# Kernel optimization log

Measured on AMD Instinct MI355X. Metric: run time of the kernel, lower is better.

The kernel has to match this reference:

```python
import jax, jax.numpy as jnp
import numpy as np

B, TQ, TK, QD, KD = 16, 256, 256, 512, 512

def setup_inputs() -> dict:
    key = jax.random.key(0)
    k = jax.random.split(key, 8)
    query = jax.random.normal(k[0], (B, TQ, QD), dtype=jnp.float32)
    keys = jax.random.normal(k[1], (B, TK, KD), dtype=jnp.float32)
    # linear_q: query_size -> key_size (stored as [in, out] for x @ W)
    Wq = jax.random.normal(k[2], (QD, KD), dtype=jnp.float32) * 0.02
    bq = jnp.zeros((KD,), dtype=jnp.float32)
    # linear_att: key_size -> 1
    w_att = jax.random.normal(k[3], (KD,), dtype=jnp.float32) * 0.02
    b_att = jnp.zeros((), dtype=jnp.float32)
    # linear_out: (query_size + key_size) -> query_size
    Wout = jax.random.normal(k[4], (QD + KD, QD), dtype=jnp.float32) * 0.02
    bout = jnp.zeros((QD,), dtype=jnp.float32)
    return {"query": query, "keys": keys, "Wq": Wq, "bq": bq,
            "w_att": w_att, "b_att": b_att, "Wout": Wout, "bout": bout}

def reference(query, keys, Wq, bq, w_att, b_att, Wout, bout):
    # att_query = linear_q(query): [b, t_q, n]
    att_query = query @ Wq + bq
    # Bahdanau additive score: tanh(q_i + k_j) . w + b  -> [b, t_q, t_k]
    sum_qk = jnp.tanh(att_query[:, :, None, :] + keys[:, None, :, :])  # b,tq,tk,n
    scores = jnp.einsum('bqkn,n->bqk', sum_qk, w_att) + b_att
    p = jax.nn.softmax(scores, axis=-1)  # softmax over t_k
    # values defaults to keys
    context = jnp.einsum('bqk,bkn->bqn', p, keys)
    # output transform: tanh(linear_out([query; context]))
    context = jnp.tanh(jnp.concatenate([query, context], axis=-1) @ Wout + bout)
    return context, p
```

## Files before the change

### kernel.cpp

```cpp
#include <hip/hip_runtime.h>


#define C2 2.88539008177792681f

typedef unsigned short u16;
typedef short s16x8 __attribute__((ext_vector_type(8)));
typedef float f32x4 __attribute__((ext_vector_type(4)));
typedef float f32x2 __attribute__((ext_vector_type(2)));

__device__ __forceinline__ float fast_rcp(float x) { return __builtin_amdgcn_rcpf(x); }
__device__ __forceinline__ f32x2 fma2(f32x2 a, f32x2 b, f32x2 c) {
  return __builtin_elementwise_fma(a, b, c);
}

__device__ __forceinline__ u16 f2bf(float f) {
  union { float f; unsigned u; } v; v.f = f;
  unsigned r = v.u + 0x7fffu + ((v.u >> 16) & 1u);
  return (u16)(r >> 16);
}
__device__ __forceinline__ unsigned packbf(float a, float b) {
  return (unsigned)f2bf(a) | ((unsigned)f2bf(b) << 16);
}

__global__ __launch_bounds__(256) void mega_prep(
    const float* __restrict__ keys, float* __restrict__ Ek,
    const float* __restrict__ query, u16* __restrict__ qbf,
    u16* __restrict__ kbfT,
    const float* __restrict__ Wq, u16* __restrict__ Wqt,
    const float* __restrict__ Wout, u16* __restrict__ Woutt,
    const float* __restrict__ w_att, const float* __restrict__ b_att,
    float* __restrict__ Cptr)
{
  __shared__ float red[4];
  __shared__ u16 tile[32][40];
  const int t = threadIdx.x;
  const int bx = blockIdx.x;

  if (bx < 2048) {
    const int b = bx >> 7, rem = bx & 127;
    const int k0 = (rem >> 4) * 32, n0 = (rem & 15) * 32;
    const float* src = keys + (size_t)b * 131072;
    const int r = t >> 3, c = (t & 7) * 4;
    const size_t off = (size_t)(k0 + r) * 512 + n0 + c;
    float4 v = *(const float4*)&src[off];
    float4 o;
    o.x = exp2f(C2 * v.x); o.y = exp2f(C2 * v.y);
    o.z = exp2f(C2 * v.z); o.w = exp2f(C2 * v.w);
    *(float4*)&Ek[(size_t)b * 131072 + off] = o;
    tile[c + 0][r] = f2bf(v.x); tile[c + 1][r] = f2bf(v.y);
    tile[c + 2][r] = f2bf(v.z); tile[c + 3][r] = f2bf(v.w);
    __syncthreads();
    if (t < 128) {
      const int row = t >> 2, ch = (t & 3) * 8;
      unsigned p0 = (unsigned)tile[row][ch + 0] | ((unsigned)tile[row][ch + 1] << 16);
      unsigned p1 = (unsigned)tile[row][ch + 2] | ((unsigned)tile[row][ch + 3] << 16);
      unsigned p2 = (unsigned)tile[row][ch + 4] | ((unsigned)tile[row][ch + 5] << 16);
      unsigned p3 = (unsigned)tile[row][ch + 6] | ((unsigned)tile[row][ch + 7] << 16);
      *(int4*)&kbfT[(size_t)b * 131072 + (size_t)(n0 + row) * 256 + k0 + ch] =
          make_int4(p0, p1, p2, p3);
    }
  } else if (bx < 3072) {
    const size_t i8 = ((size_t)(bx - 2048) * 256 + t) * 8;
    float4 a = *(const float4*)&query[i8];
    float4 b = *(const float4*)&query[i8 + 4];
    unsigned p0 = packbf(a.x, a.y), p1 = packbf(a.z, a.w);
    unsigned p2 = packbf(b.x, b.y), p3 = packbf(b.z, b.w);
    *(int4*)&qbf[i8] = make_int4(p0, p1, p2, p3);
  } else if (bx < 3840) {
    const int b3 = bx - 3072;
    const int by = b3 >> 4;
    const int n0 = (b3 & 15) * 32;
    const float* W; u16* Wt; int K, k0;
    if (by < 16) { W = Wq;   Wt = Wqt;   K = 512;  k0 = by * 32; }
    else         { W = Wout; Wt = Woutt; K = 1024; k0 = (by - 16) * 32; }
    const int r = t >> 3, c = (t & 7) * 4;
    float4 v = *(const float4*)&W[(size_t)(k0 + r) * 512 + n0 + c];
    tile[c + 0][r] = f2bf(v.x); tile[c + 1][r] = f2bf(v.y);
    tile[c + 2][r] = f2bf(v.z); tile[c + 3][r] = f2bf(v.w);
    __syncthreads();
    if (t < 128) {
      const int row = t >> 2, ch = (t & 3) * 8;
      unsigned p0 = (unsigned)tile[row][ch + 0] | ((unsigned)tile[row][ch + 1] << 16);
      unsigned p1 = (unsigned)tile[row][ch + 2] | ((unsigned)tile[row][ch + 3] << 16);
      unsigned p2 = (unsigned)tile[row][ch + 4] | ((unsigned)tile[row][ch + 5] << 16);
      unsigned p3 = (unsigned)tile[row][ch + 6] | ((unsigned)tile[row][ch + 7] << 16);
      *(int4*)&Wt[(size_t)(n0 + row) * K + k0 + ch] = make_int4(p0, p1, p2, p3);
    }
  } else {
    float wsum = w_att[t] + w_att[t + 256];
#pragma unroll
    for (int m = 32; m; m >>= 1) wsum += __shfl_xor(wsum, m);
    if ((t & 63) == 0) red[t >> 6] = wsum;
    __syncthreads();
    if (t == 0) Cptr[0] = red[0] + red[1] + red[2] + red[3] + b_att[0];
  }
}

__global__ __launch_bounds__(256) void gemm_mfma_bf16(
    const u16* __restrict__ A0, const u16* __restrict__ A1, int kSplit,
    const u16* __restrict__ Bt, const float* __restrict__ bias,
    float* __restrict__ C, int K, int act)
{
  __shared__ u16 As[64 * 72];
  __shared__ u16 Bs[64 * 72];
  const int t = threadIdx.x;
  const int lane = t & 63, wid = t >> 6;
  const int wm = wid >> 1, wn = wid & 1;
  const int col0 = blockIdx.x * 64, row0 = blockIdx.y * 64;
  const int lr = t >> 2, lc = (t & 3) * 16;
  const int fr = lane & 15, fg = (lane >> 4) * 8;

  f32x4 acc[2][2] = {};
  const int nIter = K >> 6;

  int4 a0v, a1v, b0v, b1v;
  {
    const u16* Asrc = (0 < kSplit) ? A0 : A1;
    a0v = *(const int4*)&Asrc[(size_t)(row0 + lr) * 512 + lc];
    a1v = *(const int4*)&Asrc[(size_t)(row0 + lr) * 512 + lc + 8];
    b0v = *(const int4*)&Bt[(size_t)(col0 + lr) * K + lc];
    b1v = *(const int4*)&Bt[(size_t)(col0 + lr) * K + lc + 8];
  }
  for (int it = 0; it < nIter; ++it) {
    __syncthreads();
    *(int4*)&As[lr * 72 + lc]     = a0v;
    *(int4*)&As[lr * 72 + lc + 8] = a1v;
    *(int4*)&Bs[lr * 72 + lc]     = b0v;
    *(int4*)&Bs[lr * 72 + lc + 8] = b1v;
    __syncthreads();

    if (it + 1 < nIter) {
      const int k0 = (it + 1) << 6;
      const u16* Asrc; int kc;
      if (k0 < kSplit) { Asrc = A0; kc = k0; } else { Asrc = A1; kc = k0 - kSplit; }
      a0v = *(const int4*)&Asrc[(size_t)(row0 + lr) * 512 + kc + lc];
      a1v = *(const int4*)&Asrc[(size_t)(row0 + lr) * 512 + kc + lc + 8];
      b0v = *(const int4*)&Bt[(size_t)(col0 + lr) * K + k0 + lc];
      b1v = *(const int4*)&Bt[(size_t)(col0 + lr) * K + k0 + lc + 8];
    }

#pragma unroll
    for (int ks = 0; ks < 2; ++ks) {
      s16x8 af[2], bf[2];
#pragma unroll
      for (int m = 0; m < 2; ++m)
        af[m] = *(const s16x8*)&As[(wm * 32 + m * 16 + fr) * 72 + ks * 32 + fg];
#pragma unroll
      for (int n = 0; n < 2; ++n)
        bf[n] = *(const s16x8*)&Bs[(wn * 32 + n * 16 + fr) * 72 + ks * 32 + fg];
#pragma unroll
      for (int m = 0; m < 2; ++m)
#pragma unroll
        for (int n = 0; n < 2; ++n)
          acc[m][n] = __builtin_amdgcn_mfma_f32_16x16x32_bf16(af[m], bf[n], acc[m][n], 0, 0, 0);
    }
  }

  const int fq = lane >> 4;
#pragma unroll
  for (int n = 0; n < 2; ++n) {
    const int col = col0 + wn * 32 + n * 16 + fr;
    const float bv = bias[col];
#pragma unroll
    for (int m = 0; m < 2; ++m) {
#pragma unroll
      for (int i = 0; i < 4; ++i) {
        const int row = row0 + wm * 32 + m * 16 + fq * 4 + i;
        float v = acc[m][n][i] + bv;
        if (act == 1) {
          float e = __expf(2.0f * v);
          v = 1.0f - 2.0f * fast_rcp(e + 1.0f);
        } else if (act == 2) {
          v = exp2f(C2 * v);
        }
        C[(size_t)row * 512 + col] = v;
      }
    }
  }
}

__global__ __launch_bounds__(256) void score_kernel(
    const float* __restrict__ Ea, const float* __restrict__ Ek,
    const float* __restrict__ w_att, const float* __restrict__ Cptr,
    float* __restrict__ S)
{
  __shared__ float ea_s[64][68];
  __shared__ float ek_s[64][68];

  const int z = blockIdx.z;
  const int b = z >> 2, qt = z & 3;
  const int q0 = blockIdx.y * 64, k0 = blockIdx.x * 64;
  const int t = threadIdx.x;

  const int qi = t >> 4, ki = t & 15;
  const int lr = t >> 2, lc = (t & 3) * 16;
  const float* eap = Ea + (size_t)(b * 256 + q0) * 512 + qt * 128;
  const float* ekp = Ek + (size_t)(b * 256 + k0) * 512 + qt * 128;
  const float* wbase = w_att + qt * 128;

  float acc[4][4] = {};
  const f32x2 one = {1.0f, 1.0f};

  for (int c = 0; c < 2; ++c) {
    const int gb = lr * 512 + c * 64 + lc;
    float4 A0 = *(const float4*)&eap[gb + 0];
    float4 A1 = *(const float4*)&eap[gb + 4];
    float4 A2 = *(const float4*)&eap[gb + 8];
    float4 A3 = *(const float4*)&eap[gb + 12];
    float4 K0 = *(const float4*)&ekp[gb + 0];
    float4 K1 = *(const float4*)&ekp[gb + 4];
    float4 K2 = *(const float4*)&ekp[gb + 8];
    float4 K3 = *(const float4*)&ekp[gb + 12];
    __syncthreads();
    *(float4*)&ea_s[lr][lc + 0]  = A0;
    *(float4*)&ea_s[lr][lc + 4]  = A1;
    *(float4*)&ea_s[lr][lc + 8]  = A2;
    *(float4*)&ea_s[lr][lc + 12] = A3;
    *(float4*)&ek_s[lr][lc + 0]  = K0;
    *(float4*)&ek_s[lr][lc + 4]  = K1;
    *(float4*)&ek_s[lr][lc + 8]  = K2;
    *(float4*)&ek_s[lr][lc + 12] = K3;
    __syncthreads();

    for (int j = 0; j < 64; j += 8) {
      f32x2 kp[4][4];
#pragma unroll
      for (int n = 0; n < 4; ++n) {
        float4 kv0 = *(const float4*)&ek_s[ki + n * 16][j];
        float4 kv1 = *(const float4*)&ek_s[ki + n * 16][j + 4];
        kp[n][0] = f32x2{kv0.x, kv0.y};
        kp[n][1] = f32x2{kv0.z, kv0.w};
        kp[n][2] = f32x2{kv1.x, kv1.y};
        kp[n][3] = f32x2{kv1.z, kv1.w};
      }
      const float* wq = wbase + c * 64 + j;
      f32x2 wp0 = {wq[0], wq[1]};
      f32x2 wp1 = {wq[2], wq[3]};
      f32x2 wp2 = {wq[4], wq[5]};
      f32x2 wp3 = {wq[6], wq[7]};

#pragma unroll
      for (int m = 0; m < 4; ++m) {
        float4 av0 = *(const float4*)&ea_s[qi + m * 16][j];
        float4 av1 = *(const float4*)&ea_s[qi + m * 16][j + 4];
        f32x2 ap0 = {av0.x, av0.y};
        f32x2 ap1 = {av0.z, av0.w};
        f32x2 ap2 = {av1.x, av1.y};
        f32x2 ap3 = {av1.z, av1.w};
#pragma unroll
        for (int n = 0; n < 4; ++n) {
          f32x2 q1 = fma2(ap0, kp[n][0], one);
          f32x2 q2 = fma2(ap1, kp[n][1], one);
          f32x2 q3 = fma2(ap2, kp[n][2], one);
          f32x2 q4 = fma2(ap3, kp[n][3], one);
          f32x2 N12 = fma2(wp0, q2, wp1 * q1);
          f32x2 D12 = q1 * q2;
          f32x2 N34 = fma2(wp2, q4, wp3 * q3);
          f32x2 D34 = q3 * q4;
          f32x2 Nt = fma2(N12, D34, N34 * D12);
          f32x2 Dt = D12 * D34;
          float r0 = fast_rcp(Dt.x);
          float r1 = fast_rcp(Dt.y);
          acc[m][n] = fmaf(Nt.x, r0, acc[m][n]);
          acc[m][n] = fmaf(Nt.y, r1, acc[m][n]);
        }
      }
    }
  }

  const float Cv = (qt == 0) ? Cptr[0] : 0.0f;
  float* sc = S + (size_t)qt * 1048576;
#pragma unroll
  for (int m = 0; m < 4; ++m) {
    const size_t qr = (size_t)(b * 256 + q0 + qi + m * 16);
#pragma unroll
    for (int n = 0; n < 4; ++n)
      sc[qr * 256 + k0 + ki + n * 16] = fmaf(-2.f, acc[m][n], Cv);
  }
}

__global__ __launch_bounds__(256) void softmax_kernel(
    const float* __restrict__ S, float* __restrict__ p_out,
    u16* __restrict__ pbf)
{
  const int t = threadIdx.x;
  const int w = t >> 6, lane = t & 63;
  const int row = blockIdx.x * 4 + w;
  const size_t off = (size_t)row * 256 + lane * 4;
  float4 sa = *(const float4*)&S[off];
  float4 sb = *(const float4*)&S[off + 1048576];
  float4 sc = *(const float4*)&S[off + 2097152];
  float4 sd = *(const float4*)&S[off + 3145728];
  float4 s4 = {(sa.x + sb.x) + (sc.x + sd.x), (sa.y + sb.y) + (sc.y + sd.y),
               (sa.z + sb.z) + (sc.z + sd.z), (sa.w + sb.w) + (sc.w + sd.w)};
  float m = fmaxf(fmaxf(s4.x, s4.y), fmaxf(s4.z, s4.w));
#pragma unroll
  for (int msk = 32; msk; msk >>= 1) m = fmaxf(m, __shfl_xor(m, msk));
  float e0 = __expf(s4.x - m);
  float e1 = __expf(s4.y - m);
  float e2 = __expf(s4.z - m);
  float e3 = __expf(s4.w - m);
  float ssum = (e0 + e1) + (e2 + e3);
#pragma unroll
  for (int msk = 32; msk; msk >>= 1) ssum += __shfl_xor(ssum, msk);
  float rs = 1.0f / ssum;
  float4 p4 = {e0 * rs, e1 * rs, e2 * rs, e3 * rs};
  *(float4*)&p_out[off] = p4;
  unsigned lo = packbf(p4.x, p4.y), hi = packbf(p4.z, p4.w);
  *(int2*)&pbf[off] = make_int2(lo, hi);
}

__global__ __launch_bounds__(256) void ctx_gemm(
    const u16* __restrict__ pbf, const u16* __restrict__ kbfT,
    u16* __restrict__ ctxbf)
{
  __shared__ u16 As[64 * 72];
  __shared__ u16 Bs[64 * 72];
  const int t = threadIdx.x;
  const int lane = t & 63, wid = t >> 6;
  const int wm = wid >> 1, wn = wid & 1;
  const int col0 = blockIdx.x * 64, row0 = blockIdx.y * 64, b = blockIdx.z;
  const u16* A = pbf + (size_t)b * 65536;
  const u16* Bm = kbfT + (size_t)b * 131072;
  const int lr = t >> 2, lc = (t & 3) * 16;
  const int fr = lane & 15, fg = (lane >> 4) * 8;

  f32x4 acc[2][2] = {};

  int4 a0v = *(const int4*)&A[(size_t)(row0 + lr) * 256 + lc];
  int4 a1v = *(const int4*)&A[(size_t)(row0 + lr) * 256 + lc + 8];
  int4 b0v = *(const int4*)&Bm[(size_t)(col0 + lr) * 256 + lc];
  int4 b1v = *(const int4*)&Bm[(size_t)(col0 + lr) * 256 + lc + 8];

  for (int it = 0; it < 4; ++it) {
    __syncthreads();
    *(int4*)&As[lr * 72 + lc]     = a0v;
    *(int4*)&As[lr * 72 + lc + 8] = a1v;
    *(int4*)&Bs[lr * 72 + lc]     = b0v;
    *(int4*)&Bs[lr * 72 + lc + 8] = b1v;
    __syncthreads();

    if (it < 3) {
      const int k0 = (it + 1) << 6;
      a0v = *(const int4*)&A[(size_t)(row0 + lr) * 256 + k0 + lc];
      a1v = *(const int4*)&A[(size_t)(row0 + lr) * 256 + k0 + lc + 8];
      b0v = *(const int4*)&Bm[(size_t)(col0 + lr) * 256 + k0 + lc];
      b1v = *(const int4*)&Bm[(size_t)(col0 + lr) * 256 + k0 + lc + 8];
    }

#pragma unroll
    for (int ks = 0; ks < 2; ++ks) {
      s16x8 af[2], bf[2];
#pragma unroll
      for (int m = 0; m < 2; ++m)
        af[m] = *(const s16x8*)&As[(wm * 32 + m * 16 + fr) * 72 + ks * 32 + fg];
#pragma unroll
      for (int n = 0; n < 2; ++n)
        bf[n] = *(const s16x8*)&Bs[(wn * 32 + n * 16 + fr) * 72 + ks * 32 + fg];
#pragma unroll
      for (int m = 0; m < 2; ++m)
#pragma unroll
        for (int n = 0; n < 2; ++n)
          acc[m][n] = __builtin_amdgcn_mfma_f32_16x16x32_bf16(af[m], bf[n], acc[m][n], 0, 0, 0);
    }
  }

  const int fq = lane >> 4;
#pragma unroll
  for (int n = 0; n < 2; ++n) {
    const int col = col0 + wn * 32 + n * 16 + fr;
#pragma unroll
    for (int m = 0; m < 2; ++m) {
#pragma unroll
      for (int i = 0; i < 4; ++i) {
        const int row = row0 + wm * 32 + m * 16 + fq * 4 + i;
        ctxbf[(size_t)(b * 256 + row) * 512 + col] = f2bf(acc[m][n][i]);
      }
    }
  }
}

extern "C" void kernel_launch(void* const* d_in, const int* in_sizes, int n_in,
                              void* d_out, int out_size, void* d_ws, size_t ws_size,
                              hipStream_t stream) {
  const float* query = (const float*)d_in[0];
  const float* keys  = (const float*)d_in[1];
  const float* Wq    = (const float*)d_in[2];
  const float* bq    = (const float*)d_in[3];
  const float* w_att = (const float*)d_in[4];
  const float* b_att = (const float*)d_in[5];
  const float* Wout  = (const float*)d_in[6];
  const float* bout  = (const float*)d_in[7];

  float* out_tanh = (float*)d_out;
  float* out_p    = out_tanh + (size_t)4096 * 512;

  float* ws = (float*)d_ws;
  float* Ea     = ws;
  float* Ek     = ws + 2097152;
  float* S      = ws + 4194304;
  float* Cptr   = ws + 8388608;
  u16*   Wqt    = (u16*)(ws + 8388624);
  u16*   Woutt  = Wqt + 262144;
  u16*   qbf    = Woutt + 524288;
  u16*   kbfT   = qbf + 2097152;
  u16*   pbf    = kbfT + 2097152;
  u16*   ctxbf  = (u16*)Ea;

  mega_prep<<<3841, 256, 0, stream>>>(
      keys, Ek, query, qbf, kbfT, Wq, Wqt, Wout, Woutt, w_att, b_att, Cptr);

  gemm_mfma_bf16<<<dim3(8, 64), 256, 0, stream>>>(
      qbf, qbf, 512, Wqt, bq, Ea, 512, 2);

  score_kernel<<<dim3(4, 4, 64), 256, 0, stream>>>(
      Ea, Ek, w_att, Cptr, S);

  softmax_kernel<<<1024, 256, 0, stream>>>(S, out_p, pbf);

  ctx_gemm<<<dim3(8, 4, 16), 256, 0, stream>>>(pbf, kbfT, ctxbf);

  gemm_mfma_bf16<<<dim3(8, 64), 256, 0, stream>>>(
      qbf, ctxbf, 512, Woutt, bout, out_tanh, 1024, 1);
}
```

Baseline: 100.2 us.

## Read query-side tiles directly from global memory and drop packed-float math in score kernel

The score kernel no longer stages the Ea (exp of projected query) tile in shared memory; each thread reads its query rows straight from global memory (relying on cache) while keys stay in LDS. The packed f32x2 arithmetic is replaced by scalar fmaf expressed through a macro, and w_att is loaded as float4. This cuts LDS traffic and shared-memory footprint, which may raise occupancy, at the cost of uncoalesced global loads and the loss of packed-FMA throughput on the dominant transcendental-free inner loop.

```diff
diff --git a/kernel.cpp b/kernel.cpp
--- a/kernel.cpp
+++ b/kernel.cpp
@@ -6,12 +6,8 @@
 typedef unsigned short u16;
 typedef short s16x8 __attribute__((ext_vector_type(8)));
 typedef float f32x4 __attribute__((ext_vector_type(4)));
-typedef float f32x2 __attribute__((ext_vector_type(2)));
 
 __device__ __forceinline__ float fast_rcp(float x) { return __builtin_amdgcn_rcpf(x); }
-__device__ __forceinline__ f32x2 fma2(f32x2 a, f32x2 b, f32x2 c) {
-  return __builtin_elementwise_fma(a, b, c);
-}
 
 __device__ __forceinline__ u16 f2bf(float f) {
   union { float f; unsigned u; } v; v.f = f;
@@ -184,7 +180,6 @@
     const float* __restrict__ w_att, const float* __restrict__ Cptr,
     float* __restrict__ S)
 {
-  __shared__ float ea_s[64][68];
   __shared__ float ek_s[64][68];
 
   const int z = blockIdx.z;
@@ -194,28 +189,32 @@
 
   const int qi = t >> 4, ki = t & 15;
   const int lr = t >> 2, lc = (t & 3) * 16;
-  const float* eap = Ea + (size_t)(b * 256 + q0) * 512 + qt * 128;
+  const float* eaq = Ea + (size_t)(b * 256 + q0 + qi) * 512 + qt * 128;
   const float* ekp = Ek + (size_t)(b * 256 + k0) * 512 + qt * 128;
   const float* wbase = w_att + qt * 128;
 
   float acc[4][4] = {};
-  const f32x2 one = {1.0f, 1.0f};
+
+#define TERM4(a4, kv, wv, accv) { \
+    float q1 = fmaf(a4.x, kv.x, 1.0f); \
+    float q2 = fmaf(a4.y, kv.y, 1.0f); \
+    float q3 = fmaf(a4.z, kv.z, 1.0f); \
+    float q4 = fmaf(a4.w, kv.w, 1.0f); \
+    float N12 = fmaf(wv.x, q2, wv.y * q1); \
+    float D12 = q1 * q2; \
+    float N34 = fmaf(wv.z, q4, wv.w * q3); \
+    float D34 = q3 * q4; \
+    float Nt = fmaf(N12, D34, N34 * D12); \
+    float Dt = D12 * D34; \
+    accv = fmaf(Nt, fast_rcp(Dt), accv); }
 
   for (int c = 0; c < 2; ++c) {
     const int gb = lr * 512 + c * 64 + lc;
-    float4 A0 = *(const float4*)&eap[gb + 0];
-    float4 A1 = *(const float4*)&eap[gb + 4];
-    float4 A2 = *(const float4*)&eap[gb + 8];
-    float4 A3 = *(const float4*)&eap[gb + 12];
     float4 K0 = *(const float4*)&ekp[gb + 0];
     float4 K1 = *(const float4*)&ekp[gb + 4];
     float4 K2 = *(const float4*)&ekp[gb + 8];
     float4 K3 = *(const float4*)&ekp[gb + 12];
     __syncthreads();
-    *(float4*)&ea_s[lr][lc + 0]  = A0;
-    *(float4*)&ea_s[lr][lc + 4]  = A1;
-    *(float4*)&ea_s[lr][lc + 8]  = A2;
-    *(float4*)&ea_s[lr][lc + 12] = A3;
     *(float4*)&ek_s[lr][lc + 0]  = K0;
     *(float4*)&ek_s[lr][lc + 4]  = K1;
     *(float4*)&ek_s[lr][lc + 8]  = K2;
@@ -223,50 +222,28 @@
     __syncthreads();
 
     for (int j = 0; j < 64; j += 8) {
-      f32x2 kp[4][4];
+      const float* wq = wbase + c * 64 + j;
+      float4 wv0 = *(const float4*)&wq[0];
+      float4 wv1 = *(const float4*)&wq[4];
+      float4 kv0[4], kv1[4];
 #pragma unroll
       for (int n = 0; n < 4; ++n) {
-        float4 kv0 = *(const float4*)&ek_s[ki + n * 16][j];
-        float4 kv1 = *(const float4*)&ek_s[ki + n * 16][j + 4];
-        kp[n][0] = f32x2{kv0.x, kv0.y};
-        kp[n][1] = f32x2{kv0.z, kv0.w};
-        kp[n][2] = f32x2{kv1.x, kv1.y};
-        kp[n][3] = f32x2{kv1.z, kv1.w};
+        kv0[n] = *(const float4*)&ek_s[ki + n * 16][j];
+        kv1[n] = *(const float4*)&ek_s[ki + n * 16][j + 4];
       }
-      const float* wq = wbase + c * 64 + j;
-      f32x2 wp0 = {wq[0], wq[1]};
-      f32x2 wp1 = {wq[2], wq[3]};
-      f32x2 wp2 = {wq[4], wq[5]};
-      f32x2 wp3 = {wq[6], wq[7]};
-
 #pragma unroll
       for (int m = 0; m < 4; ++m) {
-        float4 av0 = *(const float4*)&ea_s[qi + m * 16][j];
-        float4 av1 = *(const float4*)&ea_s[qi + m * 16][j + 4];
-        f32x2 ap0 = {av0.x, av0.y};
-        f32x2 ap1 = {av0.z, av0.w};
-        f32x2 ap2 = {av1.x, av1.y};
-        f32x2 ap3 = {av1.z, av1.w};
+        float4 av0 = *(const float4*)&eaq[m * 16 * 512 + c * 64 + j];
+        float4 av1 = *(const float4*)&eaq[m * 16 * 512 + c * 64 + j + 4];
 #pragma unroll
         for (int n = 0; n < 4; ++n) {
-          f32x2 q1 = fma2(ap0, kp[n][0], one);
-          f32x2 q2 = fma2(ap1, kp[n][1], one);
-          f32x2 q3 = fma2(ap2, kp[n][2], one);
-          f32x2 q4 = fma2(ap3, kp[n][3], one);
-          f32x2 N12 = fma2(wp0, q2, wp1 * q1);
-          f32x2 D12 = q1 * q2;
-          f32x2 N34 = fma2(wp2, q4, wp3 * q3);
-          f32x2 D34 = q3 * q4;
-          f32x2 Nt = fma2(N12, D34, N34 * D12);
-          f32x2 Dt = D12 * D34;
-          float r0 = fast_rcp(Dt.x);
-          float r1 = fast_rcp(Dt.y);
-          acc[m][n] = fmaf(Nt.x, r0, acc[m][n]);
-          acc[m][n] = fmaf(Nt.y, r1, acc[m][n]);
+          TERM4(av0, kv0[n], wv0, acc[m][n]);
+          TERM4(av1, kv1[n], wv1, acc[m][n]);
         }
       }
     }
   }
+#undef TERM4
 
   const float Cv = (qt == 0) ? Cptr[0] : 0.0f;
   float* sc = S + (size_t)qt * 1048576;
```

Result: no change. 98.40 us (-1.8%).
